# Performance work log

Hardware: AMD Instinct MI355X
Metric: run time of the kernel (lower is better)

The kernel has to match this reference:

```python
import jax, jax.numpy as jnp
import numpy as np
import math
from jax import lax

SQRT_HALF = math.sqrt(0.5)

def _causal_dilated_conv(x, w, b, dilation):
    # x: [B, C, T], w: [O, I, K] (torch layout), causal left padding (K-1)*dilation
    k = w.shape[-1]
    pad = (k - 1) * dilation
    y = lax.conv_general_dilated(
        x, w,
        window_strides=(1,),
        padding=((pad, 0),),
        rhs_dilation=(dilation,),
        dimension_numbers=('NCH', 'OIH', 'NCH'),
    )
    return y + b[None, :, None]


def setup_inputs() -> dict:
    key = jax.random.key(0)
    ks = jax.random.split(key, 9)
    B, C, S, T, K = 8, 512, 256, 8192, 2
    scale = 1.0 / np.sqrt(C * K)
    return {
        'x': jax.random.normal(ks[0], (B, C, T), jnp.float32),
        'filter_w': jax.random.normal(ks[1], (C, C, K), jnp.float32) * scale,
        'filter_b': jax.random.normal(ks[2], (C,), jnp.float32) * scale,
        'gate_w': jax.random.normal(ks[3], (C, C, K), jnp.float32) * scale,
        'gate_b': jax.random.normal(ks[4], (C,), jnp.float32) * scale,
        'res_w': jax.random.normal(ks[5], (C, C), jnp.float32) / np.sqrt(C),
        'res_b': jax.random.normal(ks[6], (C,), jnp.float32) / np.sqrt(C),
        'skip_w': jax.random.normal(ks[7], (S, C), jnp.float32) / np.sqrt(C),
        'skip_b': jax.random.normal(ks[8], (S,), jnp.float32) / np.sqrt(C),
        'dilation': 4,
    }


def reference(x, filter_w, filter_b, gate_w, gate_b, res_w, res_b, skip_w, skip_b, dilation):
    filter_out = jnp.tanh(_causal_dilated_conv(x, filter_w, filter_b, dilation))
    gate_out = jax.nn.sigmoid(_causal_dilated_conv(x, gate_w, gate_b, dilation))
    x_gated = filter_out * gate_out  # [B, C, T]
    # 1x1 convs as channel contractions
    res_out = jnp.einsum('oc,bct->bot', res_w, x_gated) + res_b[None, :, None]
    skip_out = jnp.einsum('sc,bct->bst', skip_w, x_gated) + skip_b[None, :, None]
    return ((x + res_out) * SQRT_HALF, skip_out)
```

## Files before the change

### kernel.cpp

```cpp
#include <hip/hip_runtime.h>
#include <hip/hip_bf16.h>

typedef __attribute__((ext_vector_type(4))) float f32x4;
typedef __attribute__((ext_vector_type(8))) short bf16x8;
typedef unsigned int   u32;
typedef unsigned short u16;

#define DPAD 8
#define B_   8
#define C_   512
#define T_   8192
#define S_   256

#define OFF_WBIG 0u
#define OFF_W2   2097152u
#define OFF_B1   2883584u
#define OFF_B2   2887680u
#define OFF_XT   2891776u
#define OFF_ZT   70066176u

__device__ __forceinline__ u16 f2bf(float f) {
  u32 u = __builtin_bit_cast(u32, f);
  u += 0x7FFFu + ((u >> 16) & 1u);
  return (u16)(u >> 16);
}
__device__ __forceinline__ float sigm_(float x) { return 1.0f / (1.0f + __expf(-x)); }
__device__ __forceinline__ float tanh_(float x) { return 2.0f / (1.0f + __expf(-2.0f * x)) - 1.0f; }

__device__ __forceinline__ void gload_lds16(const void* g, void* l) {
  __builtin_amdgcn_global_load_lds(
      (const __attribute__((address_space(1))) void*)g,
      (__attribute__((address_space(3))) void*)l, 16, 0, 0);
}

__global__ void pack_kernel(const float* __restrict__ fw, const float* __restrict__ fb,
                            const float* __restrict__ gw, const float* __restrict__ gb,
                            const float* __restrict__ rw, const float* __restrict__ rb,
                            const float* __restrict__ sw, const float* __restrict__ sb,
                            u16* __restrict__ Wbig, u16* __restrict__ W2,
                            float* __restrict__ b1, float* __restrict__ b2,
                            u16* __restrict__ Xt)
{
  int idx = blockIdx.x * 256 + threadIdx.x;
  if (idx < 1048576) {
    int row = idx >> 10, k = idx & 1023;
    int i = row >> 1;
    const float* src = (row & 1) ? gw : fw;
    float v = src[((i << 9) + (k & 511)) * 2 + ((k < 512) ? 1 : 0)];
    Wbig[idx] = f2bf(v);
    return;
  }
  idx -= 1048576;
  if (idx < 393216) {
    int r = idx >> 9, k = idx & 511;
    float v = (r < 512) ? rw[(r << 9) + k] : sw[((r - 512) << 9) + k];
    W2[idx] = f2bf(v);
    return;
  }
  idx -= 393216;
  if (idx < 1024) { b1[idx] = (idx & 1) ? gb[idx >> 1] : fb[idx >> 1]; return; }
  idx -= 1024;
  if (idx < 768) { b2[idx] = (idx < 512) ? rb[idx] : sb[idx - 512]; return; }
  idx -= 768;
  if (idx < B_ * DPAD * C_) {
    int b = idx >> 12;
    int rest = idx & 4095;
    Xt[(size_t)b * (T_ + DPAD) * C_ + rest] = 0;
  }
}

__global__ __launch_bounds__(256) void transpose_kernel(const float* __restrict__ x,
                                                        u16* __restrict__ Xt)
{
  __shared__ float tile[64][65];
  int bid = blockIdx.x;
  int ct = bid & 7, tt = (bid >> 3) & 127, b = bid >> 10;
  int w = threadIdx.x >> 6, ln = threadIdx.x & 63;
  const float* xp = x + ((size_t)(b * C_ + ct * 64)) * T_ + tt * 64;
#pragma unroll
  for (int r = 0; r < 16; ++r) {
    int cl = r * 4 + w;
    tile[cl][ln] = xp[(size_t)cl * T_ + ln];
  }
  __syncthreads();
  u16* op = Xt + ((size_t)b * (T_ + DPAD) + DPAD + tt * 64) * C_ + ct * 64;
#pragma unroll
  for (int r = 0; r < 16; ++r) {
    int tl = r * 4 + w;
    op[(size_t)tl * C_ + ln] = f2bf(tile[ln][tl]);
  }
}

__global__ __launch_bounds__(512, 2) void gemm1_kernel(
    const u16* __restrict__ W, const u16* __restrict__ Xt,
    const float* __restrict__ b1, u16* __restrict__ Zt,
    const int* __restrict__ dptr)
{
  __shared__ __align__(16) u16 smem[65536];
  const int dcap = *dptr;
  const int tid = threadIdx.x;
  const int lane = tid & 63, wave = tid >> 6;
  const int wm = wave >> 2, wn = wave & 3;
  const int lp = lane & 15, lg = lane >> 4, lx = lane & 7;

  const int bid = blockIdx.x;
  const int xcd = bid & 7;
  const int idx = bid >> 3;
  const int mt  = idx & 3;
  const int nt  = (xcd << 5) | (idx >> 2);
  const int m0  = mt * 256;
  const int n0g = nt * 256;
  const int b = n0g >> 13, t0 = n0g & (T_ - 1);
  const size_t xtb = (size_t)b * (T_ + DPAD) * C_;

  const int srl = tid >> 3;
  const int skb = tid & 7;
  const int sxk = (skb ^ (srl & 7)) << 3;

  f32x4 acc[8][4];
#pragma unroll
  for (int i = 0; i < 8; ++i)
#pragma unroll
    for (int j = 0; j < 4; ++j) acc[i][j] = (f32x4){0.f, 0.f, 0.f, 0.f};

#define SQA(kt_, dd, q_) do {                                                  \
    const int row_ = (q_) * 64 + srl;                                          \
    gload_lds16(W + (size_t)(m0 + row_) * 1024 + (kt_) * 64 + sxk,             \
                smem + (dd) * 16384 + (q_) * 4096 + tid * 8);                  \
  } while (0)

#define SQB(kt_, dd, q_) do {                                                  \
    const int row_ = (q_) * 64 + srl;                                          \
    const int kg_  = (kt_) * 64 + sxk;                                         \
    const int rsh_ = (kg_ >= 512) ? dcap : 0;                                  \
    gload_lds16(Xt + xtb + (size_t)(DPAD + t0 + row_ - rsh_) * C_ + (kg_ & 511), \
                smem + 32768 + (dd) * 16384 + (q_) * 4096 + tid * 8);          \
  } while (0)

#define LDA_(Ab_, f_, kk_) \
  (*(const bf16x8*)((Ab_) + (size_t)(wm * 128 + (f_) * 16 + lp) * 64 + ((((kk_) * 4 + lg) ^ lx) << 3)))
#define LDB_(Bb_, j_, kk_) \
  (*(const bf16x8*)((Bb_) + (size_t)(wn * 64 + (j_) * 16 + lp) * 64 + ((((kk_) * 4 + lg) ^ lx) << 3)))

#define READA(a_, p_, Ab_) do {                                                \
    a_[0] = LDA_(Ab_, 2 * (p_), 0);  a_[1] = LDA_(Ab_, 2 * (p_), 1);           \
    a_[2] = LDA_(Ab_, 2 * (p_) + 1, 0); a_[3] = LDA_(Ab_, 2 * (p_) + 1, 1);    \
  } while (0)

#define MFMAPH(a_, p_) do {                                                    \
    __builtin_amdgcn_s_setprio(1);                                             \
    _Pragma("unroll") for (int kk_ = 0; kk_ < 2; ++kk_) {                      \
      _Pragma("unroll") for (int j_ = 0; j_ < 4; ++j_)                         \
        acc[2*(p_)][j_]   = __builtin_amdgcn_mfma_f32_16x16x32_bf16(a_[kk_],     bfr[j_][kk_], acc[2*(p_)][j_],   0, 0, 0); \
      _Pragma("unroll") for (int j_ = 0; j_ < 4; ++j_)                         \
        acc[2*(p_)+1][j_] = __builtin_amdgcn_mfma_f32_16x16x32_bf16(a_[2 + kk_], bfr[j_][kk_], acc[2*(p_)+1][j_], 0, 0, 0); \
    }                                                                          \
    __builtin_amdgcn_s_setprio(0);                                             \
  } while (0)

#define LGKM(n_) do { asm volatile("s_waitcnt lgkmcnt(" #n_ ")" ::: "memory"); \
                      __builtin_amdgcn_sched_barrier(0); } while (0)
#define VMW(n_)  do { asm volatile("s_waitcnt vmcnt(" #n_ ")" ::: "memory");   \
                      __builtin_amdgcn_sched_barrier(0); } while (0)

  bf16x8 bfr[4][2];
  bf16x8 aW[4], aX[4];

  SQB(0, 0, 0); SQB(0, 0, 1); SQB(0, 0, 2); SQB(0, 0, 3);
  SQA(0, 0, 0); SQA(0, 0, 1); SQA(0, 0, 2); SQA(0, 0, 3);
  VMW(0);
  __builtin_amdgcn_s_barrier();

  for (int t = 0; t < 15; ++t) {
    const int dd = t & 1, de = dd ^ 1;
    const u16* Ab = smem + dd * 16384;
    const u16* Bb = smem + 32768 + dd * 16384;
#pragma unroll
    for (int j = 0; j < 4; ++j) { bfr[j][0] = LDB_(Bb, j, 0); bfr[j][1] = LDB_(Bb, j, 1); }
    READA(aW, 0, Ab);
    READA(aX, 1, Ab);
    LGKM(4);
    MFMAPH(aW, 0);
    SQB(t + 1, de, 0); SQB(t + 1, de, 1); SQB(t + 1, de, 2); SQB(t + 1, de, 3);
    READA(aW, 2, Ab);
    LGKM(4);
    MFMAPH(aX, 1);
    SQA(t + 1, de, 0); SQA(t + 1, de, 1); SQA(t + 1, de, 2); SQA(t + 1, de, 3);
    READA(aX, 3, Ab);
    LGKM(4);
    MFMAPH(aW, 2);
    LGKM(0);
    MFMAPH(aX, 3);
    VMW(0);
    __builtin_amdgcn_s_barrier();
  }
  {
    const u16* Ab = smem + 16384;
    const u16* Bb = smem + 49152;
#pragma unroll
    for (int j = 0; j < 4; ++j) { bfr[j][0] = LDB_(Bb, j, 0); bfr[j][1] = LDB_(Bb, j, 1); }
    READA(aW, 0, Ab);
    READA(aX, 1, Ab);
    LGKM(4);
    MFMAPH(aW, 0);
    READA(aW, 2, Ab);
    LGKM(4);
    MFMAPH(aX, 1);
    READA(aX, 3, Ab);
    LGKM(4);
    MFMAPH(aW, 2);
    LGKM(0);
    MFMAPH(aX, 3);
  }

  const int g4 = lane >> 4, p = lane & 15;
#pragma unroll
  for (int i = 0; i < 8; ++i) {
    const int R = m0 + wm * 128 + i * 16 + (g4 << 2);
    const float bi0 = b1[R], bi1 = b1[R + 1], bi2 = b1[R + 2], bi3 = b1[R + 3];
    const int c0 = R >> 1;
#pragma unroll
    for (int j = 0; j < 4; ++j) {
      const int ttc = t0 + wn * 64 + j * 16 + p;
      f32x4 v = acc[i][j];
      float z0 = tanh_(v[0] + bi0) * sigm_(v[1] + bi1);
      float z1 = tanh_(v[2] + bi2) * sigm_(v[3] + bi3);
      u32 pk = (u32)f2bf(z0) | ((u32)f2bf(z1) << 16);
      *(u32*)(Zt + (size_t)(b * T_ + ttc) * C_ + c0) = pk;
    }
  }
#undef SQA
#undef SQB
#undef LDA_
#undef LDB_
#undef READA
#undef MFMAPH
#undef LGKM
#undef VMW
}

__global__ __launch_bounds__(256, 4) void gemm2_kernel(
    const u16* __restrict__ W2, const u16* __restrict__ Zt,
    const float* __restrict__ b2, const float* __restrict__ x,
    float* __restrict__ out)
{
  __shared__ __align__(16) u16 As[128 * 32];
  __shared__ __align__(16) u16 Bs[128 * 32];
  __shared__ __align__(16) float fstall[4 * 1088];
  const int tid = threadIdx.x;
  const int lane = tid & 63, wave = tid >> 6;
  const int wm = wave >> 1, wn = wave & 1;

  const int bid = blockIdx.x;
  const int xcd = bid & 7;
  const int idx = bid >> 3;
  const int mt  = idx % 6;
  const int nt  = (xcd << 6) + idx / 6;
  const int m0 = mt * 128;
  const int n0g = nt * 128;
  const int b = n0g >> 13, t0 = n0g & (T_ - 1);
  const int srow = tid >> 2;
  const int skk  = (tid & 3) * 8;

  f32x4 acc[4][4];
#pragma unroll
  for (int i = 0; i < 4; ++i)
#pragma unroll
    for (int j = 0; j < 4; ++j) acc[i][j] = (f32x4){0.f, 0.f, 0.f, 0.f};

  const int aoff = (wm * 64 + (lane & 15)) * 32 + (lane >> 4) * 8;
  const int boff = (wn * 64 + (lane & 15)) * 32 + (lane >> 4) * 8;
  const size_t ztb = (size_t)b * T_ * C_;

  for (int kc = 0; kc < 16; ++kc) {
    const int k = kc * 32 + skk;
    const u16* gA = W2 + (size_t)(m0 + srow) * 512 + k;
    const u16* gB = Zt + ztb + (size_t)(t0 + srow) * C_ + k;
    gload_lds16(gA,            As + tid * 8);
    gload_lds16(gA + 64 * 512, As + 2048 + tid * 8);
    gload_lds16(gB,            Bs + tid * 8);
    gload_lds16(gB + 64 * C_,  Bs + 2048 + tid * 8);
    asm volatile("s_waitcnt vmcnt(0)" ::: "memory");
    __syncthreads();
    bf16x8 af[4], bfr[4];
#pragma unroll
    for (int i = 0; i < 4; ++i) af[i]  = *(const bf16x8*)(As + aoff + i * 512);
#pragma unroll
    for (int j = 0; j < 4; ++j) bfr[j] = *(const bf16x8*)(Bs + boff + j * 512);
#pragma unroll
    for (int i = 0; i < 4; ++i)
#pragma unroll
      for (int j = 0; j < 4; ++j)
        acc[i][j] = __builtin_amdgcn_mfma_f32_16x16x32_bf16(af[i], bfr[j], acc[i][j], 0, 0, 0);
    __syncthreads();
  }

  float* const fst = fstall + wave * 1088;
  const int g = lane >> 4, p = lane & 15;
  const bool isres = (m0 < 512);

#pragma unroll
  for (int i = 0; i < 4; ++i) {
#pragma unroll
    for (int j = 0; j < 4; ++j)
#pragma unroll
      for (int r = 0; r < 4; ++r)
        fst[(g * 4 + r) * 68 + j * 16 + p] = acc[i][j][r];
#pragma unroll
    for (int q = 0; q < 4; ++q) {
      const int lrow = q * 4 + g;
      const int row = m0 + wm * 64 + i * 16 + lrow;
      const int t = t0 + wn * 64 + p * 4;
      f32x4 v = *(const f32x4*)&fst[lrow * 68 + p * 4];
      const float bias = b2[row];
      f32x4 res;
      if (isres) {
        const size_t o = ((size_t)(b * 512 + row)) * T_ + t;
        f32x4 xv = *(const f32x4*)(x + o);
#pragma unroll
        for (int e = 0; e < 4; ++e)
          res[e] = (xv[e] + v[e] + bias) * 0.70710678118654752f;
        *(f32x4*)(out + o) = res;
      } else {
        const size_t o = (size_t)33554432 + ((size_t)(b * 256 + (row - 512))) * T_ + t;
#pragma unroll
        for (int e = 0; e < 4; ++e)
          res[e] = v[e] + bias;
        *(f32x4*)(out + o) = res;
      }
    }
  }
}

extern "C" void kernel_launch(void* const* d_in, const int* in_sizes, int n_in,
                              void* d_out, int out_size, void* d_ws, size_t ws_size,
                              hipStream_t stream) {
  const float* x  = (const float*)d_in[0];
  const float* fw = (const float*)d_in[1];
  const float* fb = (const float*)d_in[2];
  const float* gw = (const float*)d_in[3];
  const float* gb = (const float*)d_in[4];
  const float* rw = (const float*)d_in[5];
  const float* rb = (const float*)d_in[6];
  const float* sw = (const float*)d_in[7];
  const float* sb = (const float*)d_in[8];
  const int* dil  = (const int*)d_in[9];

  char* ws = (char*)d_ws;
  u16*   Wbig = (u16*)(ws + OFF_WBIG);
  u16*   W2   = (u16*)(ws + OFF_W2);
  float* b1   = (float*)(ws + OFF_B1);
  float* b2   = (float*)(ws + OFF_B2);
  u16*   Xt   = (u16*)(ws + OFF_XT);
  u16*   Zt   = (u16*)(ws + OFF_ZT);
  float* out  = (float*)d_out;

  hipLaunchKernelGGL(pack_kernel, dim3(5767), dim3(256), 0, stream,
                     fw, fb, gw, gb, rw, rb, sw, sb, Wbig, W2, b1, b2, Xt);
  hipLaunchKernelGGL(transpose_kernel, dim3(8192), dim3(256), 0, stream, x, Xt);
  hipLaunchKernelGGL(gemm1_kernel, dim3(1024), dim3(512), 0, stream, Wbig, Xt, b1, Zt, dil);
  hipLaunchKernelGGL(gemm2_kernel, dim3(3072), dim3(256), 0, stream, W2, Zt, b2, x, out);
}
```

Measured before the change: 307.4 us.

## Double-buffer gemm2 K-loop and stage gemm1 Zt stores through LDS

In gemm2 the K loop now double-buffers the A and B tiles in LDS. The next chunk's global-to-LDS loads are issued before the MFMAs on the current chunk, with raised wave priority during the MFMAs, and one barrier per iteration instead of two. In gemm1's epilogue the packed bf16 gated outputs are first written to a per-wave LDS tile and then stored to Zt as contiguous rows, replacing the scattered 4-byte stores. This trades extra LDS traffic and a barrier for better coalescing and overlap of loads with compute. The gemm2 LDS layout is unified into one buffer that is reused for the epilogue.

```diff
diff --git a/kernel.cpp b/kernel.cpp
--- a/kernel.cpp
+++ b/kernel.cpp
@@ -213,21 +213,30 @@
     MFMAPH(aX, 3);
   }
 
+  __syncthreads();
+  u16* const wt = smem + wave * 4608;
   const int g4 = lane >> 4, p = lane & 15;
 #pragma unroll
   for (int i = 0; i < 8; ++i) {
     const int R = m0 + wm * 128 + i * 16 + (g4 << 2);
     const float bi0 = b1[R], bi1 = b1[R + 1], bi2 = b1[R + 2], bi3 = b1[R + 3];
-    const int c0 = R >> 1;
+    const int cl = i * 8 + g4 * 2;
 #pragma unroll
     for (int j = 0; j < 4; ++j) {
-      const int ttc = t0 + wn * 64 + j * 16 + p;
       f32x4 v = acc[i][j];
       float z0 = tanh_(v[0] + bi0) * sigm_(v[1] + bi1);
       float z1 = tanh_(v[2] + bi2) * sigm_(v[3] + bi3);
       u32 pk = (u32)f2bf(z0) | ((u32)f2bf(z1) << 16);
-      *(u32*)(Zt + (size_t)(b * T_ + ttc) * C_ + c0) = pk;
+      *(u32*)(wt + (j * 16 + p) * 72 + cl) = pk;
     }
+  }
+  const int cg = (m0 >> 1) + wm * 64 + (lane & 31) * 2;
+  const int l5 = lane >> 5;
+#pragma unroll
+  for (int s = 0; s < 32; ++s) {
+    const int tl = s * 2 + l5;
+    u32 v = *(const u32*)(wt + tl * 72 + (lane & 31) * 2);
+    *(u32*)(Zt + (size_t)(b * T_ + t0 + wn * 64 + tl) * C_ + cg) = v;
   }
 #undef SQA
 #undef SQB
@@ -244,9 +253,7 @@
     const float* __restrict__ b2, const float* __restrict__ x,
     float* __restrict__ out)
 {
-  __shared__ __align__(16) u16 As[128 * 32];
-  __shared__ __align__(16) u16 Bs[128 * 32];
-  __shared__ __align__(16) float fstall[4 * 1088];
+  __shared__ __align__(16) u16 smem2[16384];
   const int tid = threadIdx.x;
   const int lane = tid & 63, wave = tid >> 6;
   const int wm = wave >> 1, wn = wave & 1;
@@ -272,30 +279,61 @@
   const int boff = (wn * 64 + (lane & 15)) * 32 + (lane >> 4) * 8;
   const size_t ztb = (size_t)b * T_ * C_;
 
-  for (int kc = 0; kc < 16; ++kc) {
-    const int k = kc * 32 + skk;
-    const u16* gA = W2 + (size_t)(m0 + srow) * 512 + k;
-    const u16* gB = Zt + ztb + (size_t)(t0 + srow) * C_ + k;
-    gload_lds16(gA,            As + tid * 8);
-    gload_lds16(gA + 64 * 512, As + 2048 + tid * 8);
-    gload_lds16(gB,            Bs + tid * 8);
-    gload_lds16(gB + 64 * C_,  Bs + 2048 + tid * 8);
-    asm volatile("s_waitcnt vmcnt(0)" ::: "memory");
-    __syncthreads();
+  u16* const As[2] = { smem2,        smem2 + 4096 };
+  u16* const Bs[2] = { smem2 + 8192, smem2 + 12288 };
+
+#define STAGE2(dd_, kc_) do {                                                  \
+    const int k_ = (kc_) * 32 + skk;                                           \
+    gload_lds16(W2 + (size_t)(m0 + srow) * 512 + k_,           As[dd_] + tid * 8); \
+    gload_lds16(W2 + (size_t)(m0 + 64 + srow) * 512 + k_,      As[dd_] + 2048 + tid * 8); \
+    gload_lds16(Zt + ztb + (size_t)(t0 + srow) * C_ + k_,      Bs[dd_] + tid * 8); \
+    gload_lds16(Zt + ztb + (size_t)(t0 + 64 + srow) * C_ + k_, Bs[dd_] + 2048 + tid * 8); \
+  } while (0)
+
+#define LGKM0 do { asm volatile("s_waitcnt lgkmcnt(0)" ::: "memory");          \
+                   __builtin_amdgcn_sched_barrier(0); } while (0)
+#define VMW0  do { asm volatile("s_waitcnt vmcnt(0)" ::: "memory");            \
+                   __builtin_amdgcn_sched_barrier(0); } while (0)
+
+  STAGE2(0, 0);
+  VMW0;
+  __builtin_amdgcn_s_barrier();
+
+  for (int kc = 0; kc < 15; ++kc) {
+    const int dd = kc & 1, de = dd ^ 1;
     bf16x8 af[4], bfr[4];
 #pragma unroll
-    for (int i = 0; i < 4; ++i) af[i]  = *(const bf16x8*)(As + aoff + i * 512);
-#pragma unroll
-    for (int j = 0; j < 4; ++j) bfr[j] = *(const bf16x8*)(Bs + boff + j * 512);
+    for (int i = 0; i < 4; ++i) af[i]  = *(const bf16x8*)(As[dd] + aoff + i * 512);
+#pragma unroll
+    for (int j = 0; j < 4; ++j) bfr[j] = *(const bf16x8*)(Bs[dd] + boff + j * 512);
+    STAGE2(de, kc + 1);
+    LGKM0;
+    __builtin_amdgcn_s_setprio(1);
 #pragma unroll
     for (int i = 0; i < 4; ++i)
 #pragma unroll
       for (int j = 0; j < 4; ++j)
         acc[i][j] = __builtin_amdgcn_mfma_f32_16x16x32_bf16(af[i], bfr[j], acc[i][j], 0, 0, 0);
-    __syncthreads();
-  }
-
-  float* const fst = fstall + wave * 1088;
+    __builtin_amdgcn_s_setprio(0);
+    VMW0;
+    __builtin_amdgcn_s_barrier();
+  }
+  {
+    bf16x8 af[4], bfr[4];
+#pragma unroll
+    for (int i = 0; i < 4; ++i) af[i]  = *(const bf16x8*)(As[1] + aoff + i * 512);
+#pragma unroll
+    for (int j = 0; j < 4; ++j) bfr[j] = *(const bf16x8*)(Bs[1] + boff + j * 512);
+    LGKM0;
+#pragma unroll
+    for (int i = 0; i < 4; ++i)
+#pragma unroll
+      for (int j = 0; j < 4; ++j)
+        acc[i][j] = __builtin_amdgcn_mfma_f32_16x16x32_bf16(af[i], bfr[j], acc[i][j], 0, 0, 0);
+  }
+
+  __syncthreads();
+  float* const fst = (float*)smem2 + wave * 1088;
   const int g = lane >> 4, p = lane & 15;
   const bool isres = (m0 < 512);
 
@@ -330,6 +368,9 @@
       }
     }
   }
+#undef STAGE2
+#undef LGKM0
+#undef VMW0
 }
 
 extern "C" void kernel_launch(void* const* d_in, const int* in_sizes, int n_in,
```

After: 314.6 us. +2.3%, slower.
